# Kernel tuning notes

Hardware: AMD Instinct MI355X
Metric: run time of the kernel (lower is better)

Reference implementation:

```python
import jax, jax.numpy as jnp
import numpy as np

B, TE, U, IN_DIM = 128, 2048, 256, 256  # batch, encoder_ts, units(=encoder_latdim), input_dim


def setup_inputs() -> dict:
    key = jax.random.key(0)
    ks = jax.random.split(key, 16)
    s = 0.05
    return {
        "inputs": jax.random.normal(ks[0], (B, IN_DIM), jnp.float32),
        "h_tm": jax.random.normal(ks[1], (B, U), jnp.float32),
        "x_seq": jax.random.normal(ks[2], (B, TE, U), jnp.float32),
        "V_a": jax.random.normal(ks[3], (U,), jnp.float32) * s,
        "W_a": jax.random.normal(ks[4], (U, U), jnp.float32) * s,
        "U_a": jax.random.normal(ks[5], (U, U), jnp.float32) * s,
        "b_a": jnp.zeros((U,), jnp.float32),
        "C_z": jax.random.normal(ks[6], (IN_DIM + U, U), jnp.float32) * s,
        "W_z": jax.random.normal(ks[7], (U, U), jnp.float32) * s,
        "b_z": jnp.zeros((U,), jnp.float32),
        "C_r": jax.random.normal(ks[8], (IN_DIM + U, U), jnp.float32) * s,
        "W_r": jax.random.normal(ks[9], (U, U), jnp.float32) * s,
        "b_r": jnp.zeros((U,), jnp.float32),
        "C_p": jax.random.normal(ks[10], (IN_DIM + U, U), jnp.float32) * s,
        "U_p": jax.random.normal(ks[11], (U, U), jnp.float32) * s,
        "b_p": jnp.zeros((U,), jnp.float32),
    }


def reference(inputs, h_tm, x_seq, V_a, W_a, U_a, b_a,
              C_z, W_z, b_z, C_r, W_r, b_r, C_p, U_p, b_p):
    # Additive attention over encoder timesteps.
    uxpb = jnp.einsum("bte,eu->btu", x_seq, U_a) + b_a          # [B,TE,U]
    wxstm = h_tm @ W_a                                            # [B,U]
    et = jnp.einsum("btu,u->bt", jnp.tanh(wxstm[:, None, :] + uxpb), V_a)  # [B,TE]
    # Original uses unnormalized exp / sum (no max-subtraction)
    at = jnp.exp(et)
    at = at / jnp.sum(at, axis=1, keepdims=True)                  # [B,TE]
    context = jnp.einsum("bt,bte->be", at, x_seq)                 # [B,U]
    ci = jnp.concatenate([inputs, context], axis=1)               # [B,IN+U]
    zt = jax.nn.sigmoid(h_tm @ W_z + ci @ C_z + b_z)
    rt = jax.nn.sigmoid(h_tm @ W_r + ci @ C_r + b_r)
    t_ht = jnp.tanh((rt * h_tm) @ U_p + ci @ C_p + b_p)
    ht = (1.0 - zt) * h_tm + zt * t_ht
    return ht
```

## Files before the change

### kernel.cpp

```cpp
#include <hip/hip_runtime.h>

#define BB 128
#define TE 2048
#define UU 256
#define IN_DIM 256
#define MC 64
#define TCH (TE / MC)

typedef float f32x4 __attribute__((ext_vector_type(4)));
typedef short bf16x8 __attribute__((ext_vector_type(8)));
typedef unsigned short u16x4 __attribute__((ext_vector_type(4)));

__device__ __forceinline__ unsigned short f2bf(float f) {
  unsigned u = __float_as_uint(f);
  u += 0x7fffu + ((u >> 16) & 1u);
  return (unsigned short)(u >> 16);
}
__device__ __forceinline__ float bf2f(unsigned short s) {
  return __uint_as_float(((unsigned)s) << 16);
}
__device__ __forceinline__ float fast_tanh(float x) {
  float e = __expf(2.f * x);
  return 1.f - 2.f / (e + 1.f);
}
__device__ __forceinline__ float fast_sigmoid(float x) {
  return 1.f / (1.f + __expf(-x));
}

__global__ __launch_bounds__(256) void prep_kernel(
    const float* __restrict__ h_tm, const float* __restrict__ W_a,
    const float* __restrict__ b_a, const float* __restrict__ U_a,
    float* __restrict__ addvec, unsigned short* __restrict__ UaT) {
  int t = threadIdx.x;
  if (blockIdx.x < BB) {
    int bi = blockIdx.x;
    __shared__ float hL[UU];
    hL[t] = h_tm[bi * UU + t];
    __syncthreads();
    float s = b_a[t];
    for (int e = 0; e < UU; ++e) s += hL[e] * W_a[e * UU + t];
    addvec[bi * UU + t] = s;
  } else {
    int idx = (blockIdx.x - BB) * 256 + t;
    int n = idx >> 6;
    int k0 = (idx & 63) << 2;
    u16x4 pkt;
    pkt.x = f2bf(U_a[(k0 + 0) * UU + n]);
    pkt.y = f2bf(U_a[(k0 + 1) * UU + n]);
    pkt.z = f2bf(U_a[(k0 + 2) * UU + n]);
    pkt.w = f2bf(U_a[(k0 + 3) * UU + n]);
    *(u16x4*)(UaT + n * UU + k0) = pkt;
  }
}

__global__ __launch_bounds__(256) void attn_main(
    const float* __restrict__ x_seq, const float* __restrict__ V_a,
    const unsigned short* __restrict__ UaT, const float* __restrict__ addvec,
    float* __restrict__ numw, float* __restrict__ denw) {
  __shared__ __align__(16) unsigned char Xb[MC * 512];
  __shared__ float avL[UU];
  __shared__ float vaL[UU];
  __shared__ float wsum[4][MC];
  __shared__ float eL[MC];

  const int tid = threadIdx.x;
  const int bi = blockIdx.x / TCH;
  const int c = blockIdx.x % TCH;

  const float* xc = x_seq + (size_t)(bi * TE + c * MC) * UU;

#pragma unroll
  for (int i = 0; i < 16; ++i) {
    int f4 = i * 256 + tid;
    int m = f4 >> 6;
    int k = (f4 & 63) << 2;
    f32x4 v = *(const f32x4*)(xc + (size_t)f4 * 4);
    u16x4 pkt;
    pkt.x = f2bf(v.x);
    pkt.y = f2bf(v.y);
    pkt.z = f2bf(v.z);
    pkt.w = f2bf(v.w);
    int woff = m * 512 + ((k << 1) ^ ((m & 7) << 4));
    *(u16x4*)(Xb + woff) = pkt;
  }
  avL[tid] = addvec[bi * UU + tid];
  vaL[tid] = V_a[tid];
  __syncthreads();

  const int w = tid >> 6;
  const int l = tid & 63;
  const int lr = l & 15;
  const int lg = l >> 4;
  const int n0 = w * 64;

  f32x4 acc[4][4];
#pragma unroll
  for (int mi = 0; mi < 4; ++mi)
#pragma unroll
    for (int ni = 0; ni < 4; ++ni) acc[mi][ni] = (f32x4)0.f;

#pragma unroll
  for (int ks = 0; ks < 8; ++ks) {
    bf16x8 a[4], b[4];
#pragma unroll
    for (int ni = 0; ni < 4; ++ni) {
      int n = n0 + ni * 16 + lr;
      b[ni] = *(const bf16x8*)(UaT + n * UU + ks * 32 + lg * 8);
    }
#pragma unroll
    for (int mi = 0; mi < 4; ++mi) {
      int m = mi * 16 + lr;
      int off = m * 512 + ((ks * 64 + lg * 16) ^ ((m & 7) << 4));
      a[mi] = *(const bf16x8*)(Xb + off);
    }
#pragma unroll
    for (int mi = 0; mi < 4; ++mi)
#pragma unroll
      for (int ni = 0; ni < 4; ++ni)
        acc[mi][ni] =
            __builtin_amdgcn_mfma_f32_16x16x32_bf16(a[mi], b[ni], acc[mi][ni], 0, 0, 0);
  }

  float psum[4][4];
#pragma unroll
  for (int mi = 0; mi < 4; ++mi)
#pragma unroll
    for (int r = 0; r < 4; ++r) psum[mi][r] = 0.f;

#pragma unroll
  for (int ni = 0; ni < 4; ++ni) {
    int n = n0 + ni * 16 + lr;
    float av = avL[n];
    float va = vaL[n];
#pragma unroll
    for (int mi = 0; mi < 4; ++mi)
#pragma unroll
      for (int r = 0; r < 4; ++r)
        psum[mi][r] += fast_tanh(acc[mi][ni][r] + av) * va;
  }
#pragma unroll
  for (int off = 1; off < 16; off <<= 1)
#pragma unroll
    for (int mi = 0; mi < 4; ++mi)
#pragma unroll
      for (int r = 0; r < 4; ++r) psum[mi][r] += __shfl_xor(psum[mi][r], off, 64);

  if (lr == 0) {
#pragma unroll
    for (int mi = 0; mi < 4; ++mi)
#pragma unroll
      for (int r = 0; r < 4; ++r) wsum[w][mi * 16 + lg * 4 + r] = psum[mi][r];
  }
  __syncthreads();

  if (tid < MC) {
    float et = wsum[0][tid] + wsum[1][tid] + wsum[2][tid] + wsum[3][tid];
    eL[tid] = __expf(et);
  }
  __syncthreads();

  if (tid == 0) {
    float d = 0.f;
    for (int m = 0; m < MC; ++m) d += eL[m];
    denw[bi * TCH + c] = d;
  }
  float s = 0.f;
  const int sw_n = tid << 1;
#pragma unroll 8
  for (int m = 0; m < MC; ++m) {
    int off = m * 512 + (sw_n ^ ((m & 7) << 4));
    s += eL[m] * bf2f(*(const unsigned short*)(Xb + off));
  }
  numw[(bi * TCH + c) * UU + tid] = s;
}

__global__ __launch_bounds__(256) void finalize_kernel(
    const float* __restrict__ inputs, const float* __restrict__ h_tm,
    const float* __restrict__ numw, const float* __restrict__ denw,
    const float* __restrict__ C_z, const float* __restrict__ W_z,
    const float* __restrict__ b_z, const float* __restrict__ C_r,
    const float* __restrict__ W_r, const float* __restrict__ b_r,
    const float* __restrict__ C_p, const float* __restrict__ U_p,
    const float* __restrict__ b_p, float* __restrict__ out) {
  int bi = blockIdx.x, t = threadIdx.x;
  __shared__ float hL[UU], ciL[IN_DIM + UU], rhL[UU];
  float ns = 0.f;
#pragma unroll 4
  for (int c = 0; c < TCH; ++c) ns += numw[(bi * TCH + c) * UU + t];
  float ds = 0.f;
  for (int c = 0; c < TCH; ++c) ds += denw[bi * TCH + c];
  ciL[IN_DIM + t] = ns / ds;
  ciL[t] = inputs[bi * IN_DIM + t];
  hL[t] = h_tm[bi * UU + t];
  __syncthreads();

  float z = b_z[t], r = b_r[t], p = b_p[t];
  for (int e = 0; e < UU; ++e) {
    float h = hL[e];
    z += h * W_z[e * UU + t];
    r += h * W_r[e * UU + t];
  }
  for (int e = 0; e < IN_DIM + UU; ++e) {
    float cv = ciL[e];
    z += cv * C_z[e * UU + t];
    r += cv * C_r[e * UU + t];
    p += cv * C_p[e * UU + t];
  }
  z = fast_sigmoid(z);
  r = fast_sigmoid(r);
  rhL[t] = r * hL[t];
  __syncthreads();
  for (int e = 0; e < UU; ++e) p += rhL[e] * U_p[e * UU + t];
  float th = fast_tanh(p);
  out[bi * UU + t] = (1.f - z) * hL[t] + z * th;
}

extern "C" void kernel_launch(void* const* d_in, const int* in_sizes, int n_in,
                              void* d_out, int out_size, void* d_ws, size_t ws_size,
                              hipStream_t stream) {
  const float* inputs = (const float*)d_in[0];
  const float* h_tm = (const float*)d_in[1];
  const float* x_seq = (const float*)d_in[2];
  const float* V_a = (const float*)d_in[3];
  const float* W_a = (const float*)d_in[4];
  const float* U_a = (const float*)d_in[5];
  const float* b_a = (const float*)d_in[6];
  const float* C_z = (const float*)d_in[7];
  const float* W_z = (const float*)d_in[8];
  const float* b_z = (const float*)d_in[9];
  const float* C_r = (const float*)d_in[10];
  const float* W_r = (const float*)d_in[11];
  const float* b_r = (const float*)d_in[12];
  const float* C_p = (const float*)d_in[13];
  const float* U_p = (const float*)d_in[14];
  const float* b_p = (const float*)d_in[15];

  unsigned short* UaT = (unsigned short*)d_ws;
  float* addvec = (float*)((char*)d_ws + 131072);
  float* numw = (float*)((char*)d_ws + 262144);
  float* denw = (float*)((char*)d_ws + 262144 + 4194304);
  float* out = (float*)d_out;

  prep_kernel<<<BB + 64, 256, 0, stream>>>(h_tm, W_a, b_a, U_a, addvec, UaT);
  attn_main<<<BB * TCH, 256, 0, stream>>>(x_seq, V_a, UaT, addvec, numw, denw);
  finalize_kernel<<<BB, 256, 0, stream>>>(inputs, h_tm, numw, denw, C_z, W_z, b_z, C_r,
                                          W_r, b_r, C_p, U_p, b_p, out);
}
```

Before: 513.3 us.

## Persistent double-buffered attention loop with fp16 MFMA and split-K finalize

The attention kernel now has each block walk eight 32-row chunks of x_seq. Rows are staged in fp32 through double-buffered LDS with register prefetch, and the U_a fragments are held in registers across chunks. Activations are converted to fp16 on the fly for f16 MFMA, replacing the bf16 pre-conversion, and the context numerator and denominator are accumulated across chunks. This shrinks the partial buffers and the number of blocks. Finalize moves to 1024 threads with a 4-way split over the reduction dimension of the gate matvecs, which adds register pressure and extra LDS reduction steps.

```diff
diff --git a/kernel.cpp b/kernel.cpp
--- a/kernel.cpp
+++ b/kernel.cpp
@@ -4,21 +4,14 @@
 #define TE 2048
 #define UU 256
 #define IN_DIM 256
-#define MC 64
-#define TCH (TE / MC)
+#define MC 32
+#define NCH 8
+#define GPB 8
 
 typedef float f32x4 __attribute__((ext_vector_type(4)));
-typedef short bf16x8 __attribute__((ext_vector_type(8)));
-typedef unsigned short u16x4 __attribute__((ext_vector_type(4)));
-
-__device__ __forceinline__ unsigned short f2bf(float f) {
-  unsigned u = __float_as_uint(f);
-  u += 0x7fffu + ((u >> 16) & 1u);
-  return (unsigned short)(u >> 16);
-}
-__device__ __forceinline__ float bf2f(unsigned short s) {
-  return __uint_as_float(((unsigned)s) << 16);
-}
+typedef __fp16 f16x2 __attribute__((ext_vector_type(2)));
+typedef _Float16 f16x8 __attribute__((ext_vector_type(8)));
+
 __device__ __forceinline__ float fast_tanh(float x) {
   float e = __expf(2.f * x);
   return 1.f - 2.f / (e + 1.f);
@@ -26,11 +19,15 @@
 __device__ __forceinline__ float fast_sigmoid(float x) {
   return 1.f / (1.f + __expf(-x));
 }
+__device__ __forceinline__ void bar_lds() {
+  asm volatile("s_waitcnt lgkmcnt(0)" ::: "memory");
+  __builtin_amdgcn_s_barrier();
+}
 
 __global__ __launch_bounds__(256) void prep_kernel(
     const float* __restrict__ h_tm, const float* __restrict__ W_a,
     const float* __restrict__ b_a, const float* __restrict__ U_a,
-    float* __restrict__ addvec, unsigned short* __restrict__ UaT) {
+    float* __restrict__ addvec, _Float16* __restrict__ UhT2) {
   int t = threadIdx.x;
   if (blockIdx.x < BB) {
     int bi = blockIdx.x;
@@ -41,140 +38,155 @@
     for (int e = 0; e < UU; ++e) s += hL[e] * W_a[e * UU + t];
     addvec[bi * UU + t] = s;
   } else {
-    int idx = (blockIdx.x - BB) * 256 + t;
-    int n = idx >> 6;
-    int k0 = (idx & 63) << 2;
-    u16x4 pkt;
-    pkt.x = f2bf(U_a[(k0 + 0) * UU + n]);
-    pkt.y = f2bf(U_a[(k0 + 1) * UU + n]);
-    pkt.z = f2bf(U_a[(k0 + 2) * UU + n]);
-    pkt.w = f2bf(U_a[(k0 + 3) * UU + n]);
-    *(u16x4*)(UaT + n * UU + k0) = pkt;
-  }
-}
-
-__global__ __launch_bounds__(256) void attn_main(
+    int b2 = blockIdx.x - BB;
+    int n = t;
+    union { f16x8 v; _Float16 h[8]; } pk;
+#pragma unroll
+    for (int e = 0; e < 8; ++e) pk.h[e] = (_Float16)U_a[(b2 * 8 + e) * UU + n];
+    *(f16x8*)(UhT2 + ((b2 * UU + n) << 3)) = pk.v;
+  }
+}
+
+__global__ __launch_bounds__(256, 2) void attn_main(
     const float* __restrict__ x_seq, const float* __restrict__ V_a,
-    const unsigned short* __restrict__ UaT, const float* __restrict__ addvec,
+    const _Float16* __restrict__ UhT2, const float* __restrict__ addvec,
     float* __restrict__ numw, float* __restrict__ denw) {
-  __shared__ __align__(16) unsigned char Xb[MC * 512];
-  __shared__ float avL[UU];
-  __shared__ float vaL[UU];
+  __shared__ __align__(16) float Xb[2][MC * UU];
+  __shared__ float avL[UU], vaL[UU];
   __shared__ float wsum[4][MC];
   __shared__ float eL[MC];
 
   const int tid = threadIdx.x;
-  const int bi = blockIdx.x / TCH;
-  const int c = blockIdx.x % TCH;
-
-  const float* xc = x_seq + (size_t)(bi * TE + c * MC) * UU;
-
-#pragma unroll
-  for (int i = 0; i < 16; ++i) {
-    int f4 = i * 256 + tid;
-    int m = f4 >> 6;
-    int k = (f4 & 63) << 2;
-    f32x4 v = *(const f32x4*)(xc + (size_t)f4 * 4);
-    u16x4 pkt;
-    pkt.x = f2bf(v.x);
-    pkt.y = f2bf(v.y);
-    pkt.z = f2bf(v.z);
-    pkt.w = f2bf(v.w);
-    int woff = m * 512 + ((k << 1) ^ ((m & 7) << 4));
-    *(u16x4*)(Xb + woff) = pkt;
-  }
+  const int bi = blockIdx.x >> 3;
+  const int g = blockIdx.x & 7;
+  const float* xc = x_seq + (size_t)(bi * TE + g * (MC * NCH)) * UU;
+
+  const int w = tid >> 6, l = tid & 63, lr = l & 15, lg = l >> 4;
+  const int rlow = lr & 7;
+
+  f32x4 st[8];
+#pragma unroll
+  for (int j = 0; j < 8; ++j) st[j] = *(const f32x4*)(xc + (size_t)(j * 256 + tid) * 4);
+
   avL[tid] = addvec[bi * UU + tid];
   vaL[tid] = V_a[tid];
-  __syncthreads();
-
-  const int w = tid >> 6;
-  const int l = tid & 63;
-  const int lr = l & 15;
-  const int lg = l >> 4;
-  const int n0 = w * 64;
-
-  f32x4 acc[4][4];
-#pragma unroll
-  for (int mi = 0; mi < 4; ++mi)
-#pragma unroll
-    for (int ni = 0; ni < 4; ++ni) acc[mi][ni] = (f32x4)0.f;
-
-#pragma unroll
-  for (int ks = 0; ks < 8; ++ks) {
-    bf16x8 a[4], b[4];
+
+  f16x8 Bf[8][4];
+#pragma unroll
+  for (int ks = 0; ks < 8; ++ks)
 #pragma unroll
     for (int ni = 0; ni < 4; ++ni) {
-      int n = n0 + ni * 16 + lr;
-      b[ni] = *(const bf16x8*)(UaT + n * UU + ks * 32 + lg * 8);
-    }
-#pragma unroll
-    for (int mi = 0; mi < 4; ++mi) {
-      int m = mi * 16 + lr;
-      int off = m * 512 + ((ks * 64 + lg * 16) ^ ((m & 7) << 4));
-      a[mi] = *(const bf16x8*)(Xb + off);
-    }
-#pragma unroll
-    for (int mi = 0; mi < 4; ++mi)
-#pragma unroll
-      for (int ni = 0; ni < 4; ++ni)
-        acc[mi][ni] =
-            __builtin_amdgcn_mfma_f32_16x16x32_bf16(a[mi], b[ni], acc[mi][ni], 0, 0, 0);
-  }
-
-  float psum[4][4];
-#pragma unroll
-  for (int mi = 0; mi < 4; ++mi)
-#pragma unroll
-    for (int r = 0; r < 4; ++r) psum[mi][r] = 0.f;
-
-#pragma unroll
-  for (int ni = 0; ni < 4; ++ni) {
-    int n = n0 + ni * 16 + lr;
-    float av = avL[n];
-    float va = vaL[n];
-#pragma unroll
-    for (int mi = 0; mi < 4; ++mi)
-#pragma unroll
-      for (int r = 0; r < 4; ++r)
-        psum[mi][r] += fast_tanh(acc[mi][ni][r] + av) * va;
-  }
-#pragma unroll
-  for (int off = 1; off < 16; off <<= 1)
-#pragma unroll
-    for (int mi = 0; mi < 4; ++mi)
-#pragma unroll
-      for (int r = 0; r < 4; ++r) psum[mi][r] += __shfl_xor(psum[mi][r], off, 64);
-
-  if (lr == 0) {
-#pragma unroll
-    for (int mi = 0; mi < 4; ++mi)
-#pragma unroll
-      for (int r = 0; r < 4; ++r) wsum[w][mi * 16 + lg * 4 + r] = psum[mi][r];
-  }
-  __syncthreads();
-
-  if (tid < MC) {
-    float et = wsum[0][tid] + wsum[1][tid] + wsum[2][tid] + wsum[3][tid];
-    eL[tid] = __expf(et);
-  }
-  __syncthreads();
-
-  if (tid == 0) {
-    float d = 0.f;
-    for (int m = 0; m < MC; ++m) d += eL[m];
-    denw[bi * TCH + c] = d;
-  }
-  float s = 0.f;
-  const int sw_n = tid << 1;
+      int n = w * 64 + ni * 16 + lr;
+      Bf[ks][ni] = *(const f16x8*)(UhT2 + (((ks * 4 + lg) * UU + n) << 3));
+    }
+
+  {
+    float* B0 = &Xb[0][0];
+#pragma unroll
+    for (int j = 0; j < 8; ++j) {
+      int row = j * 4 + (tid >> 6), u = tid & 63;
+      *(f32x4*)(B0 + (((row << 6) + (u ^ (row & 7))) << 2)) = st[j];
+    }
+  }
+#pragma unroll
+  for (int j = 0; j < 8; ++j)
+    st[j] = *(const f32x4*)(xc + (size_t)(MC * UU) + (size_t)(j * 256 + tid) * 4);
+  bar_lds();
+
+  float num_acc = 0.f, den_acc = 0.f;
+  for (int i = 0; i < NCH; ++i) {
+    const float* Xc = &Xb[i & 1][0];
+    f32x4 acc[2][4];
+#pragma unroll
+    for (int mi = 0; mi < 2; ++mi)
+#pragma unroll
+      for (int ni = 0; ni < 4; ++ni) acc[mi][ni] = (f32x4)0.f;
+
+#pragma unroll
+    for (int ks = 0; ks < 8; ++ks) {
+      f16x8 a[2];
+#pragma unroll
+      for (int mi = 0; mi < 2; ++mi) {
+        const int rowoff = (mi * 16 + lr) << 8;
+        int u0 = ks * 8 + lg * 2;
+        f32x4 f0 = *(const f32x4*)(Xc + rowoff + ((u0 ^ rlow) << 2));
+        f32x4 f1 = *(const f32x4*)(Xc + rowoff + (((u0 + 1) ^ rlow) << 2));
+        union { f16x8 v; f16x2 p[4]; } A;
+        A.p[0] = __builtin_amdgcn_cvt_pkrtz(f0.x, f0.y);
+        A.p[1] = __builtin_amdgcn_cvt_pkrtz(f0.z, f0.w);
+        A.p[2] = __builtin_amdgcn_cvt_pkrtz(f1.x, f1.y);
+        A.p[3] = __builtin_amdgcn_cvt_pkrtz(f1.z, f1.w);
+        a[mi] = A.v;
+      }
+#pragma unroll
+      for (int mi = 0; mi < 2; ++mi)
+#pragma unroll
+        for (int ni = 0; ni < 4; ++ni)
+          acc[mi][ni] = __builtin_amdgcn_mfma_f32_16x16x32_f16(a[mi], Bf[ks][ni],
+                                                               acc[mi][ni], 0, 0, 0);
+    }
+
+    float psum[2][4];
+#pragma unroll
+    for (int mi = 0; mi < 2; ++mi)
+#pragma unroll
+      for (int r = 0; r < 4; ++r) psum[mi][r] = 0.f;
+#pragma unroll
+    for (int ni = 0; ni < 4; ++ni) {
+      int n = w * 64 + ni * 16 + lr;
+      float av = avL[n], va = vaL[n];
+#pragma unroll
+      for (int mi = 0; mi < 2; ++mi)
+#pragma unroll
+        for (int r = 0; r < 4; ++r)
+          psum[mi][r] += fast_tanh(acc[mi][ni][r] + av) * va;
+    }
+#pragma unroll
+    for (int off = 1; off < 16; off <<= 1)
+#pragma unroll
+      for (int mi = 0; mi < 2; ++mi)
+#pragma unroll
+        for (int r = 0; r < 4; ++r) psum[mi][r] += __shfl_xor(psum[mi][r], off, 64);
+    if (lr == 0) {
+#pragma unroll
+      for (int mi = 0; mi < 2; ++mi)
+#pragma unroll
+        for (int r = 0; r < 4; ++r) wsum[w][mi * 16 + lg * 4 + r] = psum[mi][r];
+    }
+    bar_lds();
+    if (tid < MC) {
+      float et = wsum[0][tid] + wsum[1][tid] + wsum[2][tid] + wsum[3][tid];
+      eL[tid] = __expf(et);
+    }
+    bar_lds();
+
 #pragma unroll 8
-  for (int m = 0; m < MC; ++m) {
-    int off = m * 512 + (sw_n ^ ((m & 7) << 4));
-    s += eL[m] * bf2f(*(const unsigned short*)(Xb + off));
-  }
-  numw[(bi * TCH + c) * UU + tid] = s;
-}
-
-__global__ __launch_bounds__(256) void finalize_kernel(
+    for (int m = 0; m < MC; ++m) {
+      float e = eL[m];
+      num_acc += e * Xc[(m << 8) + ((((tid >> 2) ^ (m & 7))) << 2) + (tid & 3)];
+      den_acc += e;
+    }
+
+    if (i < NCH - 1) {
+      float* Bn = &Xb[(i + 1) & 1][0];
+#pragma unroll
+      for (int j = 0; j < 8; ++j) {
+        int row = j * 4 + (tid >> 6), u = tid & 63;
+        *(f32x4*)(Bn + (((row << 6) + (u ^ (row & 7))) << 2)) = st[j];
+      }
+      if (i < NCH - 2) {
+        const float* src = xc + (size_t)(i + 2) * (MC * UU);
+#pragma unroll
+        for (int j = 0; j < 8; ++j) st[j] = *(const f32x4*)(src + (size_t)(j * 256 + tid) * 4);
+      }
+      bar_lds();
+    }
+  }
+  numw[(bi * GPB + g) * UU + tid] = num_acc;
+  if (tid == 0) denw[bi * GPB + g] = den_acc;
+}
+
+__global__ __launch_bounds__(1024) void finalize_kernel(
     const float* __restrict__ inputs, const float* __restrict__ h_tm,
     const float* __restrict__ numw, const float* __restrict__ denw,
     const float* __restrict__ C_z, const float* __restrict__ W_z,
@@ -182,37 +194,60 @@
     const float* __restrict__ W_r, const float* __restrict__ b_r,
     const float* __restrict__ C_p, const float* __restrict__ U_p,
     const float* __restrict__ b_p, float* __restrict__ out) {
-  int bi = blockIdx.x, t = threadIdx.x;
+  int bi = blockIdx.x, tid = threadIdx.x;
+  int t = tid & 255, s = tid >> 8;
   __shared__ float hL[UU], ciL[IN_DIM + UU], rhL[UU];
-  float ns = 0.f;
-#pragma unroll 4
-  for (int c = 0; c < TCH; ++c) ns += numw[(bi * TCH + c) * UU + t];
-  float ds = 0.f;
-  for (int c = 0; c < TCH; ++c) ds += denw[bi * TCH + c];
-  ciL[IN_DIM + t] = ns / ds;
-  ciL[t] = inputs[bi * IN_DIM + t];
-  hL[t] = h_tm[bi * UU + t];
-  __syncthreads();
-
-  float z = b_z[t], r = b_r[t], p = b_p[t];
-  for (int e = 0; e < UU; ++e) {
+  __shared__ float zp[4][UU], rp[4][UU], pp[4][UU];
+
+  if (s == 0) {
+    float ns = 0.f;
+#pragma unroll
+    for (int c = 0; c < GPB; ++c) ns += numw[(bi * GPB + c) * UU + t];
+    float ds = 0.f;
+#pragma unroll
+    for (int c = 0; c < GPB; ++c) ds += denw[bi * GPB + c];
+    ciL[IN_DIM + t] = ns / ds;
+    ciL[t] = inputs[bi * IN_DIM + t];
+    hL[t] = h_tm[bi * UU + t];
+  }
+  __syncthreads();
+
+  float z = 0.f, r = 0.f, p = 0.f;
+  for (int e = s * 64; e < s * 64 + 64; ++e) {
     float h = hL[e];
     z += h * W_z[e * UU + t];
     r += h * W_r[e * UU + t];
   }
-  for (int e = 0; e < IN_DIM + UU; ++e) {
+  for (int e = s * 128; e < s * 128 + 128; ++e) {
     float cv = ciL[e];
     z += cv * C_z[e * UU + t];
     r += cv * C_r[e * UU + t];
     p += cv * C_p[e * UU + t];
   }
-  z = fast_sigmoid(z);
-  r = fast_sigmoid(r);
-  rhL[t] = r * hL[t];
-  __syncthreads();
-  for (int e = 0; e < UU; ++e) p += rhL[e] * U_p[e * UU + t];
-  float th = fast_tanh(p);
-  out[bi * UU + t] = (1.f - z) * hL[t] + z * th;
+  zp[s][t] = z; rp[s][t] = r; pp[s][t] = p;
+  __syncthreads();
+
+  if (s == 0) {
+    float zz = zp[0][t] + zp[1][t] + zp[2][t] + zp[3][t] + b_z[t];
+    float rr = rp[0][t] + rp[1][t] + rp[2][t] + rp[3][t] + b_r[t];
+    zz = fast_sigmoid(zz);
+    rr = fast_sigmoid(rr);
+    zp[0][t] = zz;
+    rhL[t] = rr * hL[t];
+  }
+  __syncthreads();
+
+  float p2 = 0.f;
+  for (int e = s * 64; e < s * 64 + 64; ++e) p2 += rhL[e] * U_p[e * UU + t];
+  pp[s][t] += p2;
+  __syncthreads();
+
+  if (s == 0) {
+    float pt = pp[0][t] + pp[1][t] + pp[2][t] + pp[3][t] + b_p[t];
+    float th = fast_tanh(pt);
+    float zz = zp[0][t];
+    out[bi * UU + t] = (1.f - zz) * hL[t] + zz * th;
+  }
 }
 
 extern "C" void kernel_launch(void* const* d_in, const int* in_sizes, int n_in,
@@ -235,14 +270,14 @@
   const float* U_p = (const float*)d_in[14];
   const float* b_p = (const float*)d_in[15];
 
-  unsigned short* UaT = (unsigned short*)d_ws;
+  _Float16* UhT2 = (_Float16*)d_ws;
   float* addvec = (float*)((char*)d_ws + 131072);
   float* numw = (float*)((char*)d_ws + 262144);
-  float* denw = (float*)((char*)d_ws + 262144 + 4194304);
+  float* denw = (float*)((char*)d_ws + 262144 + 1048576);
   float* out = (float*)d_out;
 
-  prep_kernel<<<BB + 64, 256, 0, stream>>>(h_tm, W_a, b_a, U_a, addvec, UaT);
-  attn_main<<<BB * TCH, 256, 0, stream>>>(x_seq, V_a, UaT, addvec, numw, denw);
-  finalize_kernel<<<BB, 256, 0, stream>>>(inputs, h_tm, numw, denw, C_z, W_z, b_z, C_r,
-                                          W_r, b_r, C_p, U_p, b_p, out);
-}
+  prep_kernel<<<BB + 32, 256, 0, stream>>>(h_tm, W_a, b_a, U_a, addvec, UhT2);
+  attn_main<<<BB * GPB, 256, 0, stream>>>(x_seq, V_a, UhT2, addvec, numw, denw);
+  finalize_kernel<<<BB, 1024, 0, stream>>>(inputs, h_tm, numw, denw, C_z, W_z, b_z,
+                                           C_r, W_r, b_r, C_p, U_p, b_p, out);
+}
```

After: 564.2 us. 1.1x slower.
